# Kernel tuning notes

Hardware: AMD Instinct MI355X
Metric: run time of the kernel (lower is better)

## Reference

```python
import jax, jax.numpy as jnp
import numpy as np

NUM_CLASS = 1000
DIMS = 2048
NUM_HEADS = 8
HEAD = DIMS // NUM_HEADS  # 256
ALPHA = 0.999
N = 16384


def setup_inputs() -> dict:
    key = jax.random.key(0)
    k1, k2, k3 = jax.random.split(key, 3)
    x = jax.random.normal(k1, (N, DIMS), dtype=jnp.float32)
    labels = jax.random.randint(k2, (N,), 0, NUM_CLASS)
    centers = jax.random.normal(k3, (NUM_CLASS, NUM_HEADS, HEAD), dtype=jnp.float32)
    return {"x": x, "labels": labels, "centers": centers}


def reference(x, labels, centers):
    # gather per-sample centers: [N, H, hd]
    c = centers[labels]
    xh = x.reshape(-1, NUM_HEADS, HEAD)  # [N, H, hd]
    # per-head MSE, sum over heads, mean over batch
    loss = jnp.mean(jnp.square(xh - c), axis=-1).sum(axis=-1).mean()
    new_centers = centers.at[labels].set(ALPHA * c + (1.0 - ALPHA) * xh)
    return loss, new_centers
```

## Files before the change

### kernel.cpp

```cpp
#include <hip/hip_runtime.h>

#define NUM_CLASS 1000
#define DIMS 2048
#define NBATCH 16384
#define ALPHA 0.999f
#define LOSS_SCALE (1.0f / (16384.0f * 256.0f))

#define BLOCK 256
#define LOSS_BLOCKS 3096
#define TOTAL_BLOCKS (NUM_CLASS + LOSS_BLOCKS)

__global__ __launch_bounds__(BLOCK) void fused_kernel(
    const float* __restrict__ x,
    const int* __restrict__ labels,
    const float* __restrict__ centers,
    float* __restrict__ out_loss,
    float* __restrict__ newc) {
    __shared__ float smf[4];
    __shared__ int smi[4];
    const int tid  = threadIdx.x;
    const int lane = tid & 63;
    const int wid  = tid >> 6;
    const int b    = blockIdx.x;

    if (b < NUM_CLASS) {
        int best = -1;
        for (int i = tid; i < NBATCH; i += BLOCK) {
            if (labels[i] == b) best = i;
        }
        #pragma unroll
        for (int off = 32; off > 0; off >>= 1) {
            int o = __shfl_down(best, off, 64);
            best = best > o ? best : o;
        }
        if (lane == 0) smi[wid] = best;
        __syncthreads();
        if (tid == 0) {
            int v01 = smi[0] > smi[1] ? smi[0] : smi[1];
            int v23 = smi[2] > smi[3] ? smi[2] : smi[3];
            smi[0] = v01 > v23 ? v01 : v23;
        }
        __syncthreads();
        const int li = smi[0];

        const float4* crow = reinterpret_cast<const float4*>(centers + (size_t)b * DIMS);
        float* orow = newc + (size_t)b * DIMS;
        if (li >= 0) {
            const float4* xrow = reinterpret_cast<const float4*>(x + (size_t)li * DIMS);
            #pragma unroll
            for (int j = 0; j < DIMS / 4 / BLOCK; ++j) {
                int e = j * BLOCK + tid;
                float4 c4 = crow[e];
                float4 x4 = xrow[e];
                float* o = orow + e * 4;
                o[0] = ALPHA * c4.x + (1.0f - ALPHA) * x4.x;
                o[1] = ALPHA * c4.y + (1.0f - ALPHA) * x4.y;
                o[2] = ALPHA * c4.z + (1.0f - ALPHA) * x4.z;
                o[3] = ALPHA * c4.w + (1.0f - ALPHA) * x4.w;
            }
        } else {
            #pragma unroll
            for (int j = 0; j < DIMS / 4 / BLOCK; ++j) {
                int e = j * BLOCK + tid;
                float4 c4 = crow[e];
                float* o = orow + e * 4;
                o[0] = c4.x; o[1] = c4.y; o[2] = c4.z; o[3] = c4.w;
            }
        }
    } else {
        const int lb = b - NUM_CLASS;
        float acc = 0.0f;
        for (int row = lb; row < NBATCH; row += LOSS_BLOCKS) {
            const int label = labels[row];
            const float4* xr = reinterpret_cast<const float4*>(x + (size_t)row * DIMS);
            const float4* cr = reinterpret_cast<const float4*>(centers + (size_t)label * DIMS);
            #pragma unroll
            for (int j = 0; j < DIMS / 4 / BLOCK; ++j) {
                int e = j * BLOCK + tid;
                float4 xv = xr[e];
                float4 cv = cr[e];
                float dx = xv.x - cv.x;
                float dy = xv.y - cv.y;
                float dz = xv.z - cv.z;
                float dw = xv.w - cv.w;
                acc += dx * dx + dy * dy + dz * dz + dw * dw;
            }
        }
        #pragma unroll
        for (int off = 32; off > 0; off >>= 1)
            acc += __shfl_down(acc, off, 64);
        if (lane == 0) smf[wid] = acc;
        __syncthreads();
        if (tid == 0) {
            float v = (smf[0] + smf[1]) + (smf[2] + smf[3]);
            atomicAdd(out_loss, v * LOSS_SCALE);
        }
    }
}

extern "C" void kernel_launch(void* const* d_in, const int* in_sizes, int n_in,
                              void* d_out, int out_size, void* d_ws, size_t ws_size,
                              hipStream_t stream) {
    const float* x       = (const float*)d_in[0];
    const int*   labels  = (const int*)d_in[1];
    const float* centers = (const float*)d_in[2];

    float* out_loss = (float*)d_out;
    float* out_newc = (float*)d_out + 1;

    hipMemsetAsync(out_loss, 0, sizeof(float), stream);
    fused_kernel<<<TOTAL_BLOCKS, BLOCK, 0, stream>>>(x, labels, centers,
                                                     out_loss, out_newc);
}
```

Baseline: 215.3 us.

## Give every block a loss slice and overlay the center update on the first blocks

Every block now handles four contiguous batch rows of the loss reduction, and blocks below NUM_CLASS additionally do the last-writer scan and the EMA row write. This replaces the separate loss and update block groups, removing strided row assignment and the idle imbalance between the two groups. Loads of x use nontemporal hints, and the center output is written with nontemporal scalar stores to reduce cache pollution. The risk is that the first thousand blocks, which still scan all labels, become long-tail stragglers, and that the scalar nontemporal stores may not be merged into vector writes.

```diff
diff --git a/kernel.cpp b/kernel.cpp
--- a/kernel.cpp
+++ b/kernel.cpp
@@ -7,8 +7,10 @@
 #define LOSS_SCALE (1.0f / (16384.0f * 256.0f))
 
 #define BLOCK 256
-#define LOSS_BLOCKS 3096
-#define TOTAL_BLOCKS (NUM_CLASS + LOSS_BLOCKS)
+#define NBLOCKS 4096
+#define ROWS_PER_BLOCK (NBATCH / NBLOCKS)
+
+typedef float vfloat4 __attribute__((ext_vector_type(4)));
 
 __global__ __launch_bounds__(BLOCK) void fused_kernel(
     const float* __restrict__ x,
@@ -22,6 +24,33 @@
     const int lane = tid & 63;
     const int wid  = tid >> 6;
     const int b    = blockIdx.x;
+
+    float acc = 0.0f;
+    const int row0 = b * ROWS_PER_BLOCK;
+    #pragma unroll
+    for (int r = 0; r < ROWS_PER_BLOCK; ++r) {
+        const int row   = row0 + r;
+        const int label = labels[row];
+        const vfloat4* xr = reinterpret_cast<const vfloat4*>(x + (size_t)row * DIMS);
+        const vfloat4* cr = reinterpret_cast<const vfloat4*>(centers + (size_t)label * DIMS);
+        #pragma unroll
+        for (int j = 0; j < DIMS / 4 / BLOCK; ++j) {
+            const int e = j * BLOCK + tid;
+            vfloat4 xv = __builtin_nontemporal_load(xr + e);
+            vfloat4 cv = cr[e];
+            vfloat4 d = xv - cv;
+            acc += d.x * d.x + d.y * d.y + d.z * d.z + d.w * d.w;
+        }
+    }
+    #pragma unroll
+    for (int off = 32; off > 0; off >>= 1)
+        acc += __shfl_down(acc, off, 64);
+    if (lane == 0) smf[wid] = acc;
+    __syncthreads();
+    if (tid == 0) {
+        float v = (smf[0] + smf[1]) + (smf[2] + smf[3]);
+        atomicAdd(out_loss, v * LOSS_SCALE);
+    }
 
     if (b < NUM_CLASS) {
         int best = -1;
@@ -43,57 +72,32 @@
         __syncthreads();
         const int li = smi[0];
 
-        const float4* crow = reinterpret_cast<const float4*>(centers + (size_t)b * DIMS);
+        const vfloat4* crow = reinterpret_cast<const vfloat4*>(centers + (size_t)b * DIMS);
         float* orow = newc + (size_t)b * DIMS;
         if (li >= 0) {
-            const float4* xrow = reinterpret_cast<const float4*>(x + (size_t)li * DIMS);
+            const vfloat4* xrow = reinterpret_cast<const vfloat4*>(x + (size_t)li * DIMS);
             #pragma unroll
             for (int j = 0; j < DIMS / 4 / BLOCK; ++j) {
-                int e = j * BLOCK + tid;
-                float4 c4 = crow[e];
-                float4 x4 = xrow[e];
-                float* o = orow + e * 4;
-                o[0] = ALPHA * c4.x + (1.0f - ALPHA) * x4.x;
-                o[1] = ALPHA * c4.y + (1.0f - ALPHA) * x4.y;
-                o[2] = ALPHA * c4.z + (1.0f - ALPHA) * x4.z;
-                o[3] = ALPHA * c4.w + (1.0f - ALPHA) * x4.w;
+                const int e = j * BLOCK + tid;
+                vfloat4 c4 = crow[e];
+                vfloat4 x4 = xrow[e];
+                float* o = orow + (size_t)e * 4;
+                __builtin_nontemporal_store(ALPHA * c4.x + (1.0f - ALPHA) * x4.x, o + 0);
+                __builtin_nontemporal_store(ALPHA * c4.y + (1.0f - ALPHA) * x4.y, o + 1);
+                __builtin_nontemporal_store(ALPHA * c4.z + (1.0f - ALPHA) * x4.z, o + 2);
+                __builtin_nontemporal_store(ALPHA * c4.w + (1.0f - ALPHA) * x4.w, o + 3);
             }
         } else {
             #pragma unroll
             for (int j = 0; j < DIMS / 4 / BLOCK; ++j) {
-                int e = j * BLOCK + tid;
-                float4 c4 = crow[e];
-                float* o = orow + e * 4;
-                o[0] = c4.x; o[1] = c4.y; o[2] = c4.z; o[3] = c4.w;
+                const int e = j * BLOCK + tid;
+                vfloat4 c4 = crow[e];
+                float* o = orow + (size_t)e * 4;
+                __builtin_nontemporal_store(c4.x, o + 0);
+                __builtin_nontemporal_store(c4.y, o + 1);
+                __builtin_nontemporal_store(c4.z, o + 2);
+                __builtin_nontemporal_store(c4.w, o + 3);
             }
-        }
-    } else {
-        const int lb = b - NUM_CLASS;
-        float acc = 0.0f;
-        for (int row = lb; row < NBATCH; row += LOSS_BLOCKS) {
-            const int label = labels[row];
-            const float4* xr = reinterpret_cast<const float4*>(x + (size_t)row * DIMS);
-            const float4* cr = reinterpret_cast<const float4*>(centers + (size_t)label * DIMS);
-            #pragma unroll
-            for (int j = 0; j < DIMS / 4 / BLOCK; ++j) {
-                int e = j * BLOCK + tid;
-                float4 xv = xr[e];
-                float4 cv = cr[e];
-                float dx = xv.x - cv.x;
-                float dy = xv.y - cv.y;
-                float dz = xv.z - cv.z;
-                float dw = xv.w - cv.w;
-                acc += dx * dx + dy * dy + dz * dz + dw * dw;
-            }
-        }
-        #pragma unroll
-        for (int off = 32; off > 0; off >>= 1)
-            acc += __shfl_down(acc, off, 64);
-        if (lane == 0) smf[wid] = acc;
-        __syncthreads();
-        if (tid == 0) {
-            float v = (smf[0] + smf[1]) + (smf[2] + smf[3]);
-            atomicAdd(out_loss, v * LOSS_SCALE);
         }
     }
 }
@@ -108,7 +112,7 @@
     float* out_loss = (float*)d_out;
     float* out_newc = (float*)d_out + 1;
 
-    hipMemsetAsync(out_loss, 0, sizeof(float), stream);
-    fused_kernel<<<TOTAL_BLOCKS, BLOCK, 0, stream>>>(x, labels, centers,
-                                                     out_loss, out_newc);
+    (void)hipMemsetAsync(out_loss, 0, sizeof(float), stream);
+    fused_kernel<<<NBLOCKS, BLOCK, 0, stream>>>(x, labels, centers,
+                                                out_loss, out_newc);
 }
```

After: 234.0 us. 1.09x slower.
